# Kernel tuning notes

Hardware: AMD Instinct MI355X
Metric: run time of the kernel (lower is better)

Reference implementation:

```python
import jax, jax.numpy as jnp
import numpy as np

N_NODES = 100000
N_EDGES = 1600000
NFEAT, NHID, NCLASS = 64, 128, 32


def _glorot(key, shape):
    fan_in, fan_out = shape[0], shape[1]
    lim = np.sqrt(6.0 / (fan_in + fan_out))
    return jax.random.uniform(key, shape, jnp.float32, -lim, lim)


def setup_inputs() -> dict:
    key = jax.random.key(0)
    ks = jax.random.split(key, 12)
    x = jax.random.normal(ks[0], (N_NODES, NFEAT), jnp.float32)
    edge_idx = jax.random.randint(ks[1], (2, N_EDGES), 0, N_NODES, jnp.int64)
    edge_weight = jax.random.uniform(ks[2], (N_EDGES,), jnp.float32)
    return {
        "x": x,
        "edge_idx": edge_idx,
        "edge_weight": edge_weight,
        # SAGEConv 1: out = mean_agg(x) @ Wl1 + b1 + x @ Wr1
        "Wl1": _glorot(ks[3], (NFEAT, NHID)),
        "Wr1": _glorot(ks[4], (NFEAT, NHID)),
        "b1": jnp.zeros((NHID,), jnp.float32),
        # SAGEConv 2
        "Wl2": _glorot(ks[5], (NHID, NHID)),
        "Wr2": _glorot(ks[6], (NHID, NHID)),
        "b2": jnp.zeros((NHID,), jnp.float32),
        # fc head: Linear(nhid, nclass) -> Linear(nclass, 1)
        "Wfc1": _glorot(ks[7], (NHID, NCLASS)),
        "bfc1": jnp.zeros((NCLASS,), jnp.float32),
        "Wfc2": _glorot(ks[8], (NCLASS, 1)),
        "bfc2": jnp.zeros((1,), jnp.float32),
    }


def _sage_conv(x, src, dst, Wl, Wr, b, n_nodes):
    # mean aggregation of source features at destination nodes
    msg_sum = jax.ops.segment_sum(x[src], dst, num_segments=n_nodes)  # [N, d]
    deg = jax.ops.segment_sum(jnp.ones((src.shape[0], 1), x.dtype), dst,
                              num_segments=n_nodes)                    # [N, 1]
    mean = msg_sum / jnp.maximum(deg, 1.0)
    return mean @ Wl + b + x @ Wr


def reference(x, edge_idx, edge_weight, Wl1, Wr1, b1, Wl2, Wr2, b2,
              Wfc1, bfc1, Wfc2, bfc2):
    n_nodes = x.shape[0]
    src, dst = edge_idx[0], edge_idx[1]
    # dropout is identity in eval mode (training=False)
    h = _sage_conv(x, src, dst, Wl1, Wr1, b1, n_nodes)   # [N, nhid]
    h = _sage_conv(h, src, dst, Wl2, Wr2, b2, n_nodes)   # [N, nhid]
    h = h @ Wfc1 + bfc1                                   # [N, nclass]
    out = h @ Wfc2 + bfc2                                 # [N, 1]
    return out
```

## Files before the change

kernel.cpp:

```cpp
#include <hip/hip_runtime.h>

#define S_SHIFT 7
#define S_NODES 128
#define NBKT    784
#define CAP     2560
#define CHUNK   4096
#define NREP    4
#define TPB     256
#define TOTAL_BLOCKS 1024

__global__ __launch_bounds__(512) void prep_kernel(
    const float* __restrict__ Wl1, const float* __restrict__ Wr1, const float* __restrict__ b1,
    const float* __restrict__ Wl2, const float* __restrict__ Wr2, const float* __restrict__ b2,
    const float* __restrict__ Wfc1, const float* __restrict__ bfc1,
    const float* __restrict__ Wfc2, const float* __restrict__ bfc2,
    int* __restrict__ cursor, float* __restrict__ wv_g, float* __restrict__ c01)
{
    __shared__ float wv[192], uu[128], vl2[128], vr2[128], w2[32];
    int t = threadIdx.x;
    int l = t & 63;
    int w = t >> 6;
    for (int i = t; i < NBKT; i += 512) cursor[i] = 0;
    if (t < 32) w2[t] = Wfc2[t];
    __syncthreads();
    for (int j = 0; j < 16; ++j) {
        int i = w + 8 * j;
        float p = (l < 32) ? Wfc1[i * 32 + l] * w2[l] : 0.f;
        for (int m = 16; m; m >>= 1) p += __shfl_xor(p, m);
        if (l == 0) uu[i] = p;
    }
    __syncthreads();
    for (int j = 0; j < 16; ++j) {
        int i = w + 8 * j;
        float ua = uu[l], ub = uu[64 + l];
        float pa = Wl2[i * 128 + l] * ua + Wl2[i * 128 + 64 + l] * ub;
        float pb = Wr2[i * 128 + l] * ua + Wr2[i * 128 + 64 + l] * ub;
        for (int m = 32; m; m >>= 1) { pa += __shfl_xor(pa, m); pb += __shfl_xor(pb, m); }
        if (l == 0) { vl2[i] = pa; vr2[i] = pb; }
    }
    __syncthreads();
    for (int j = 0; j < 8; ++j) {
        int i = w + 8 * j;
        float l1a = Wl1[i * 128 + l], l1b = Wl1[i * 128 + 64 + l];
        float r1a = Wr1[i * 128 + l], r1b = Wr1[i * 128 + 64 + l];
        float La = vl2[l], Lb = vl2[64 + l], Ra = vr2[l], Rb = vr2[64 + l];
        float pc = l1a * La + l1b * Lb;
        float pb = l1a * Ra + l1b * Rb + r1a * La + r1b * Lb;
        float pa = r1a * Ra + r1b * Rb;
        for (int m = 32; m; m >>= 1) {
            pa += __shfl_xor(pa, m); pb += __shfl_xor(pb, m); pc += __shfl_xor(pc, m);
        }
        if (l == 0) { wv[i] = pa; wv[64 + i] = pb; wv[128 + i] = pc; }
    }
    if (w == 7) {
        float p0 = b1[l] * vr2[l] + b1[64 + l] * vr2[64 + l]
                 + b2[l] * uu[l] + b2[64 + l] * uu[64 + l];
        if (l < 32) p0 += bfc1[l] * w2[l];
        float p1 = b1[l] * vl2[l] + b1[64 + l] * vl2[64 + l];
        for (int m = 32; m; m >>= 1) { p0 += __shfl_xor(p0, m); p1 += __shfl_xor(p1, m); }
        if (l == 0) { c01[0] = p0 + bfc2[0]; c01[1] = p1; }
    }
    __syncthreads();
    for (int i = t; i < 192; i += 512) wv_g[i] = wv[i];
}

__global__ __launch_bounds__(TPB) void fused_kernel(
    const float* __restrict__ x,
    const int* __restrict__ src, const int* __restrict__ dst,
    int E, int N, int B, int nscat, int ndot,
    int* __restrict__ cursor, unsigned* __restrict__ bucket,
    const float* __restrict__ wv_g,
    float* __restrict__ ga, float2* __restrict__ gbc)
{
    __shared__ int hist[NBKT], lbase[NBKT], lcur[NBKT];
    int t = threadIdx.x;
    int l = t & 63;
    int w = t >> 6;
    int bid = blockIdx.x;

    if (bid < nscat) {
        int e0 = bid * CHUNK;
        int cnt = E - e0; if (cnt > CHUNK) cnt = CHUNK;
        for (int i = t; i < B; i += TPB) hist[i] = 0;
        __syncthreads();
        for (int i = t; i < cnt; i += TPB)
            atomicAdd(&hist[dst[e0 + i] >> S_SHIFT], 1);
        __syncthreads();
        for (int i = t; i < B; i += TPB) {
            lcur[i] = 0;
            if (hist[i] > 0) lbase[i] = atomicAdd(&cursor[i], hist[i]);
        }
        __syncthreads();
        for (int i = t; i < cnt; i += TPB) {
            int d = dst[e0 + i], s = src[e0 + i];
            int bb = d >> S_SHIFT;
            int off = atomicAdd(&lcur[bb], 1);
            bucket[(size_t)bb * CAP + (unsigned)(lbase[bb] + off)] =
                ((unsigned)s << S_SHIFT) | (unsigned)(d & (S_NODES - 1));
        }
    } else {
        int fp = l & 15, sub = l >> 4;
        float4 wa4 = ((const float4*)wv_g)[fp];
        float4 wb4 = ((const float4*)wv_g)[16 + fp];
        float4 wc4 = ((const float4*)wv_g)[32 + fp];
        const float4* x4 = (const float4*)x;
        int Q = (N + 3) >> 2;
        int wid = (bid - nscat) * (TPB / 64) + w;
        int stride = ndot * (TPB / 64);
        for (int qd = wid; qd < Q; qd += stride) {
            int node = qd * 4 + sub;
            float a = 0.f, b = 0.f, c = 0.f;
            if (node < N) {
                float4 v = x4[(size_t)node * 16 + fp];
                a = v.x * wa4.x + v.y * wa4.y + v.z * wa4.z + v.w * wa4.w;
                b = v.x * wb4.x + v.y * wb4.y + v.z * wb4.z + v.w * wb4.w;
                c = v.x * wc4.x + v.y * wc4.y + v.z * wc4.z + v.w * wc4.w;
            }
            for (int m = 8; m; m >>= 1) {
                a += __shfl_xor(a, m); b += __shfl_xor(b, m); c += __shfl_xor(c, m);
            }
            if (fp == 0 && node < N) { ga[node] = a; gbc[node] = make_float2(b, c); }
        }
    }
}

__global__ __launch_bounds__(TPB) void aggA_kernel(
    const unsigned* __restrict__ bucket, const int* __restrict__ cursor,
    const float2* __restrict__ gbc, const float* __restrict__ ga,
    const float* __restrict__ c01,
    float* __restrict__ q, float* __restrict__ t1, float* __restrict__ inv, int N)
{
    __shared__ float aB[NREP][S_NODES], aC[NREP][S_NODES];
    __shared__ int cnt[NREP][S_NODES];
    int t = threadIdx.x, b = blockIdx.x;
    int r = t >> 6;
    float* aBf = (float*)aB; float* aCf = (float*)aC; int* cnf = (int*)cnt;
    for (int i = t; i < NREP * S_NODES; i += TPB) { aBf[i] = 0.f; aCf[i] = 0.f; cnf[i] = 0; }
    __syncthreads();
    int n = cursor[b];
    const unsigned* bp = bucket + (size_t)b * CAP;
    int n4 = n & ~3;
    for (int i = 4 * t; i < n4; i += 4 * TPB) {
        uint4 e4 = *(const uint4*)(bp + i);
        float2 g0 = gbc[e4.x >> S_SHIFT];
        float2 g1 = gbc[e4.y >> S_SHIFT];
        float2 g2 = gbc[e4.z >> S_SHIFT];
        float2 g3 = gbc[e4.w >> S_SHIFT];
        int d0 = e4.x & (S_NODES - 1), d1 = e4.y & (S_NODES - 1);
        int d2 = e4.z & (S_NODES - 1), d3 = e4.w & (S_NODES - 1);
        atomicAdd(&aB[r][d0], g0.x); atomicAdd(&aC[r][d0], g0.y); atomicAdd(&cnt[r][d0], 1);
        atomicAdd(&aB[r][d1], g1.x); atomicAdd(&aC[r][d1], g1.y); atomicAdd(&cnt[r][d1], 1);
        atomicAdd(&aB[r][d2], g2.x); atomicAdd(&aC[r][d2], g2.y); atomicAdd(&cnt[r][d2], 1);
        atomicAdd(&aB[r][d3], g3.x); atomicAdd(&aC[r][d3], g3.y); atomicAdd(&cnt[r][d3], 1);
    }
    if (n4 + t < n) {
        unsigned uu = bp[n4 + t];
        float2 g = gbc[uu >> S_SHIFT];
        int dl = uu & (S_NODES - 1);
        atomicAdd(&aB[r][dl], g.x); atomicAdd(&aC[r][dl], g.y); atomicAdd(&cnt[r][dl], 1);
    }
    __syncthreads();
    if (t < S_NODES) {
        int node = (b << S_SHIFT) + t;
        if (node < N) {
            float sb = 0.f, sc = 0.f; int d = 0;
            #pragma unroll
            for (int k = 0; k < NREP; ++k) { sb += aB[k][t]; sc += aC[k][t]; d += cnt[k][t]; }
            float iv = 1.0f / ((d > 0) ? (float)d : 1.0f);
            inv[node] = iv;
            q[node]   = iv * sc;
            t1[node]  = ga[node] + iv * sb + c01[0] + (d > 0 ? c01[1] : 0.f);
        }
    }
}

__global__ __launch_bounds__(TPB) void aggB_kernel(
    const unsigned* __restrict__ bucket, const int* __restrict__ cursor,
    const float* __restrict__ q, const float* __restrict__ t1,
    const float* __restrict__ inv, float* __restrict__ out, int N)
{
    __shared__ float a2[NREP][S_NODES];
    int t = threadIdx.x, b = blockIdx.x;
    int r = t >> 6;
    float* a2f = (float*)a2;
    for (int i = t; i < NREP * S_NODES; i += TPB) a2f[i] = 0.f;
    __syncthreads();
    int n = cursor[b];
    const unsigned* bp = bucket + (size_t)b * CAP;
    int n4 = n & ~3;
    for (int i = 4 * t; i < n4; i += 4 * TPB) {
        uint4 e4 = *(const uint4*)(bp + i);
        float q0 = q[e4.x >> S_SHIFT], q1 = q[e4.y >> S_SHIFT];
        float q2 = q[e4.z >> S_SHIFT], q3 = q[e4.w >> S_SHIFT];
        atomicAdd(&a2[r][e4.x & (S_NODES - 1)], q0);
        atomicAdd(&a2[r][e4.y & (S_NODES - 1)], q1);
        atomicAdd(&a2[r][e4.z & (S_NODES - 1)], q2);
        atomicAdd(&a2[r][e4.w & (S_NODES - 1)], q3);
    }
    if (n4 + t < n) {
        unsigned uu = bp[n4 + t];
        atomicAdd(&a2[r][uu & (S_NODES - 1)], q[uu >> S_SHIFT]);
    }
    __syncthreads();
    if (t < S_NODES) {
        int node = (b << S_SHIFT) + t;
        if (node < N) {
            float s2 = 0.f;
            #pragma unroll
            for (int k = 0; k < NREP; ++k) s2 += a2[k][t];
            out[node] = t1[node] + inv[node] * s2;
        }
    }
}

extern "C" void kernel_launch(void* const* d_in, const int* in_sizes, int n_in,
                              void* d_out, int out_size, void* d_ws, size_t ws_size,
                              hipStream_t stream) {
    const float* x    = (const float*)d_in[0];
    const int*   eidx = (const int*)d_in[1];
    const float* Wl1  = (const float*)d_in[3];
    const float* Wr1  = (const float*)d_in[4];
    const float* b1   = (const float*)d_in[5];
    const float* Wl2  = (const float*)d_in[6];
    const float* Wr2  = (const float*)d_in[7];
    const float* b2   = (const float*)d_in[8];
    const float* Wfc1 = (const float*)d_in[9];
    const float* bfc1 = (const float*)d_in[10];
    const float* Wfc2 = (const float*)d_in[11];
    const float* bfc2 = (const float*)d_in[12];

    const int N = in_sizes[0] / 64;
    const int E = in_sizes[2];
    const int* src = eidx;
    const int* dst = eidx + E;
    const int B = (N + S_NODES - 1) >> S_SHIFT;
    const int nscat = (E + CHUNK - 1) / CHUNK;
    const int ndot = TOTAL_BLOCKS - nscat;

    char* ws = (char*)d_ws;
    int*      cursor = (int*)(ws);
    float*    wv_g   = (float*)(ws + 3136);
    float*    c01    = (float*)(ws + 3904);
    float*    ga     = (float*)(ws + 4096);
    float*    q      = (float*)(ws + 4096 + (size_t)N * 4);
    float*    t1     = (float*)(ws + 4096 + (size_t)N * 8);
    float*    inv    = (float*)(ws + 4096 + (size_t)N * 12);
    float2*   gbc    = (float2*)(ws + 4096 + (size_t)N * 16);
    unsigned* bucket = (unsigned*)(ws + 4096 + (size_t)N * 24);

    prep_kernel<<<1, 512, 0, stream>>>(Wl1, Wr1, b1, Wl2, Wr2, b2,
                                       Wfc1, bfc1, Wfc2, bfc2, cursor, wv_g, c01);

    fused_kernel<<<TOTAL_BLOCKS, TPB, 0, stream>>>(
        x, src, dst, E, N, B, nscat, ndot, cursor, bucket, wv_g, ga, gbc);

    aggA_kernel<<<B, TPB, 0, stream>>>(bucket, cursor, gbc, ga, c01, q, t1, inv, N);
    aggB_kernel<<<B, TPB, 0, stream>>>(bucket, cursor, q, t1, inv, (float*)d_out, N);
}
```

Before: 182.3 us.

## Fold weight-prep into fused kernel, memset cursors, prefetch bucket loads

Removes the single-block prep kernel. Every dot-product block now recomputes the collapsed weight vectors redundantly in shared memory, and the cursor reset becomes a memset. This cuts one serial launch and its tail latency, at the cost of repeated small matrix reductions per block. It also doubles the scatter chunk size, halving the number of scatter blocks, and adds one-ahead software prefetching of bucket entries in both aggregation kernels.

```diff
diff --git a/kernel.cpp b/kernel.cpp
--- a/kernel.cpp
+++ b/kernel.cpp
@@ -4,75 +4,25 @@
 #define S_NODES 128
 #define NBKT    784
 #define CAP     2560
-#define CHUNK   4096
+#define CHUNK   8192
 #define NREP    4
 #define TPB     256
 #define TOTAL_BLOCKS 1024
-
-__global__ __launch_bounds__(512) void prep_kernel(
-    const float* __restrict__ Wl1, const float* __restrict__ Wr1, const float* __restrict__ b1,
-    const float* __restrict__ Wl2, const float* __restrict__ Wr2, const float* __restrict__ b2,
-    const float* __restrict__ Wfc1, const float* __restrict__ bfc1,
-    const float* __restrict__ Wfc2, const float* __restrict__ bfc2,
-    int* __restrict__ cursor, float* __restrict__ wv_g, float* __restrict__ c01)
-{
-    __shared__ float wv[192], uu[128], vl2[128], vr2[128], w2[32];
-    int t = threadIdx.x;
-    int l = t & 63;
-    int w = t >> 6;
-    for (int i = t; i < NBKT; i += 512) cursor[i] = 0;
-    if (t < 32) w2[t] = Wfc2[t];
-    __syncthreads();
-    for (int j = 0; j < 16; ++j) {
-        int i = w + 8 * j;
-        float p = (l < 32) ? Wfc1[i * 32 + l] * w2[l] : 0.f;
-        for (int m = 16; m; m >>= 1) p += __shfl_xor(p, m);
-        if (l == 0) uu[i] = p;
-    }
-    __syncthreads();
-    for (int j = 0; j < 16; ++j) {
-        int i = w + 8 * j;
-        float ua = uu[l], ub = uu[64 + l];
-        float pa = Wl2[i * 128 + l] * ua + Wl2[i * 128 + 64 + l] * ub;
-        float pb = Wr2[i * 128 + l] * ua + Wr2[i * 128 + 64 + l] * ub;
-        for (int m = 32; m; m >>= 1) { pa += __shfl_xor(pa, m); pb += __shfl_xor(pb, m); }
-        if (l == 0) { vl2[i] = pa; vr2[i] = pb; }
-    }
-    __syncthreads();
-    for (int j = 0; j < 8; ++j) {
-        int i = w + 8 * j;
-        float l1a = Wl1[i * 128 + l], l1b = Wl1[i * 128 + 64 + l];
-        float r1a = Wr1[i * 128 + l], r1b = Wr1[i * 128 + 64 + l];
-        float La = vl2[l], Lb = vl2[64 + l], Ra = vr2[l], Rb = vr2[64 + l];
-        float pc = l1a * La + l1b * Lb;
-        float pb = l1a * Ra + l1b * Rb + r1a * La + r1b * Lb;
-        float pa = r1a * Ra + r1b * Rb;
-        for (int m = 32; m; m >>= 1) {
-            pa += __shfl_xor(pa, m); pb += __shfl_xor(pb, m); pc += __shfl_xor(pc, m);
-        }
-        if (l == 0) { wv[i] = pa; wv[64 + i] = pb; wv[128 + i] = pc; }
-    }
-    if (w == 7) {
-        float p0 = b1[l] * vr2[l] + b1[64 + l] * vr2[64 + l]
-                 + b2[l] * uu[l] + b2[64 + l] * uu[64 + l];
-        if (l < 32) p0 += bfc1[l] * w2[l];
-        float p1 = b1[l] * vl2[l] + b1[64 + l] * vl2[64 + l];
-        for (int m = 32; m; m >>= 1) { p0 += __shfl_xor(p0, m); p1 += __shfl_xor(p1, m); }
-        if (l == 0) { c01[0] = p0 + bfc2[0]; c01[1] = p1; }
-    }
-    __syncthreads();
-    for (int i = t; i < 192; i += 512) wv_g[i] = wv[i];
-}
 
 __global__ __launch_bounds__(TPB) void fused_kernel(
     const float* __restrict__ x,
     const int* __restrict__ src, const int* __restrict__ dst,
     int E, int N, int B, int nscat, int ndot,
     int* __restrict__ cursor, unsigned* __restrict__ bucket,
-    const float* __restrict__ wv_g,
-    float* __restrict__ ga, float2* __restrict__ gbc)
+    const float* __restrict__ Wl1, const float* __restrict__ Wr1, const float* __restrict__ b1,
+    const float* __restrict__ Wl2, const float* __restrict__ Wr2, const float* __restrict__ b2,
+    const float* __restrict__ Wfc1, const float* __restrict__ bfc1,
+    const float* __restrict__ Wfc2, const float* __restrict__ bfc2,
+    float* __restrict__ ga, float2* __restrict__ gbc, float* __restrict__ c01)
 {
     __shared__ int hist[NBKT], lbase[NBKT], lcur[NBKT];
+    __shared__ __align__(16) float wv[192];
+    __shared__ float uu[128], vl2[128], vr2[128], w2[32];
     int t = threadIdx.x;
     int l = t & 63;
     int w = t >> 6;
@@ -99,10 +49,51 @@
                 ((unsigned)s << S_SHIFT) | (unsigned)(d & (S_NODES - 1));
         }
     } else {
+        if (t < 32) w2[t] = Wfc2[t];
+        __syncthreads();
+        for (int j = 0; j < 32; ++j) {
+            int i = w + 4 * j;
+            float p = (l < 32) ? Wfc1[i * 32 + l] * w2[l] : 0.f;
+            for (int m = 16; m; m >>= 1) p += __shfl_xor(p, m);
+            if (l == 0) uu[i] = p;
+        }
+        __syncthreads();
+        for (int j = 0; j < 32; ++j) {
+            int i = w + 4 * j;
+            float ua = uu[l], ub = uu[64 + l];
+            float pa = Wl2[i * 128 + l] * ua + Wl2[i * 128 + 64 + l] * ub;
+            float pb = Wr2[i * 128 + l] * ua + Wr2[i * 128 + 64 + l] * ub;
+            for (int m = 32; m; m >>= 1) { pa += __shfl_xor(pa, m); pb += __shfl_xor(pb, m); }
+            if (l == 0) { vl2[i] = pa; vr2[i] = pb; }
+        }
+        __syncthreads();
+        for (int j = 0; j < 16; ++j) {
+            int i = w + 4 * j;
+            float l1a = Wl1[i * 128 + l], l1b = Wl1[i * 128 + 64 + l];
+            float r1a = Wr1[i * 128 + l], r1b = Wr1[i * 128 + 64 + l];
+            float La = vl2[l], Lb = vl2[64 + l], Ra = vr2[l], Rb = vr2[64 + l];
+            float pc = l1a * La + l1b * Lb;
+            float pb = l1a * Ra + l1b * Rb + r1a * La + r1b * Lb;
+            float pa = r1a * Ra + r1b * Rb;
+            for (int m = 32; m; m >>= 1) {
+                pa += __shfl_xor(pa, m); pb += __shfl_xor(pb, m); pc += __shfl_xor(pc, m);
+            }
+            if (l == 0) { wv[i] = pa; wv[64 + i] = pb; wv[128 + i] = pc; }
+        }
+        if (bid == nscat && w == 3) {
+            float p0 = b1[l] * vr2[l] + b1[64 + l] * vr2[64 + l]
+                     + b2[l] * uu[l] + b2[64 + l] * uu[64 + l];
+            if (l < 32) p0 += bfc1[l] * w2[l];
+            float p1 = b1[l] * vl2[l] + b1[64 + l] * vl2[64 + l];
+            for (int m = 32; m; m >>= 1) { p0 += __shfl_xor(p0, m); p1 += __shfl_xor(p1, m); }
+            if (l == 0) { c01[0] = p0 + bfc2[0]; c01[1] = p1; }
+        }
+        __syncthreads();
+
         int fp = l & 15, sub = l >> 4;
-        float4 wa4 = ((const float4*)wv_g)[fp];
-        float4 wb4 = ((const float4*)wv_g)[16 + fp];
-        float4 wc4 = ((const float4*)wv_g)[32 + fp];
+        float4 wa4 = ((const float4*)wv)[fp];
+        float4 wb4 = ((const float4*)wv)[16 + fp];
+        float4 wc4 = ((const float4*)wv)[32 + fp];
         const float4* x4 = (const float4*)x;
         int Q = (N + 3) >> 2;
         int wid = (bid - nscat) * (TPB / 64) + w;
@@ -140,18 +131,26 @@
     int n = cursor[b];
     const unsigned* bp = bucket + (size_t)b * CAP;
     int n4 = n & ~3;
-    for (int i = 4 * t; i < n4; i += 4 * TPB) {
-        uint4 e4 = *(const uint4*)(bp + i);
-        float2 g0 = gbc[e4.x >> S_SHIFT];
-        float2 g1 = gbc[e4.y >> S_SHIFT];
-        float2 g2 = gbc[e4.z >> S_SHIFT];
-        float2 g3 = gbc[e4.w >> S_SHIFT];
-        int d0 = e4.x & (S_NODES - 1), d1 = e4.y & (S_NODES - 1);
-        int d2 = e4.z & (S_NODES - 1), d3 = e4.w & (S_NODES - 1);
+    int i = 4 * t;
+    bool have = i < n4;
+    uint4 cur = make_uint4(0, 0, 0, 0);
+    if (have) cur = *(const uint4*)(bp + i);
+    while (have) {
+        int in2 = i + 4 * TPB;
+        bool hn = in2 < n4;
+        uint4 nxt = cur;
+        if (hn) nxt = *(const uint4*)(bp + in2);
+        float2 g0 = gbc[cur.x >> S_SHIFT];
+        float2 g1 = gbc[cur.y >> S_SHIFT];
+        float2 g2 = gbc[cur.z >> S_SHIFT];
+        float2 g3 = gbc[cur.w >> S_SHIFT];
+        int d0 = cur.x & (S_NODES - 1), d1 = cur.y & (S_NODES - 1);
+        int d2 = cur.z & (S_NODES - 1), d3 = cur.w & (S_NODES - 1);
         atomicAdd(&aB[r][d0], g0.x); atomicAdd(&aC[r][d0], g0.y); atomicAdd(&cnt[r][d0], 1);
         atomicAdd(&aB[r][d1], g1.x); atomicAdd(&aC[r][d1], g1.y); atomicAdd(&cnt[r][d1], 1);
         atomicAdd(&aB[r][d2], g2.x); atomicAdd(&aC[r][d2], g2.y); atomicAdd(&cnt[r][d2], 1);
         atomicAdd(&aB[r][d3], g3.x); atomicAdd(&aC[r][d3], g3.y); atomicAdd(&cnt[r][d3], 1);
+        cur = nxt; i = in2; have = hn;
     }
     if (n4 + t < n) {
         unsigned uu = bp[n4 + t];
@@ -188,14 +187,22 @@
     int n = cursor[b];
     const unsigned* bp = bucket + (size_t)b * CAP;
     int n4 = n & ~3;
-    for (int i = 4 * t; i < n4; i += 4 * TPB) {
-        uint4 e4 = *(const uint4*)(bp + i);
-        float q0 = q[e4.x >> S_SHIFT], q1 = q[e4.y >> S_SHIFT];
-        float q2 = q[e4.z >> S_SHIFT], q3 = q[e4.w >> S_SHIFT];
-        atomicAdd(&a2[r][e4.x & (S_NODES - 1)], q0);
-        atomicAdd(&a2[r][e4.y & (S_NODES - 1)], q1);
-        atomicAdd(&a2[r][e4.z & (S_NODES - 1)], q2);
-        atomicAdd(&a2[r][e4.w & (S_NODES - 1)], q3);
+    int i = 4 * t;
+    bool have = i < n4;
+    uint4 cur = make_uint4(0, 0, 0, 0);
+    if (have) cur = *(const uint4*)(bp + i);
+    while (have) {
+        int in2 = i + 4 * TPB;
+        bool hn = in2 < n4;
+        uint4 nxt = cur;
+        if (hn) nxt = *(const uint4*)(bp + in2);
+        float q0 = q[cur.x >> S_SHIFT], q1 = q[cur.y >> S_SHIFT];
+        float q2 = q[cur.z >> S_SHIFT], q3 = q[cur.w >> S_SHIFT];
+        atomicAdd(&a2[r][cur.x & (S_NODES - 1)], q0);
+        atomicAdd(&a2[r][cur.y & (S_NODES - 1)], q1);
+        atomicAdd(&a2[r][cur.z & (S_NODES - 1)], q2);
+        atomicAdd(&a2[r][cur.w & (S_NODES - 1)], q3);
+        cur = nxt; i = in2; have = hn;
     }
     if (n4 + t < n) {
         unsigned uu = bp[n4 + t];
@@ -239,8 +246,7 @@
 
     char* ws = (char*)d_ws;
     int*      cursor = (int*)(ws);
-    float*    wv_g   = (float*)(ws + 3136);
-    float*    c01    = (float*)(ws + 3904);
+    float*    c01    = (float*)(ws + 3200);
     float*    ga     = (float*)(ws + 4096);
     float*    q      = (float*)(ws + 4096 + (size_t)N * 4);
     float*    t1     = (float*)(ws + 4096 + (size_t)N * 8);
@@ -248,11 +254,12 @@
     float2*   gbc    = (float2*)(ws + 4096 + (size_t)N * 16);
     unsigned* bucket = (unsigned*)(ws + 4096 + (size_t)N * 24);
 
-    prep_kernel<<<1, 512, 0, stream>>>(Wl1, Wr1, b1, Wl2, Wr2, b2,
-                                       Wfc1, bfc1, Wfc2, bfc2, cursor, wv_g, c01);
+    hipMemsetAsync(cursor, 0, 3136, stream);
 
     fused_kernel<<<TOTAL_BLOCKS, TPB, 0, stream>>>(
-        x, src, dst, E, N, B, nscat, ndot, cursor, bucket, wv_g, ga, gbc);
+        x, src, dst, E, N, B, nscat, ndot, cursor, bucket,
+        Wl1, Wr1, b1, Wl2, Wr2, b2, Wfc1, bfc1, Wfc2, bfc2,
+        ga, gbc, c01);
 
     aggA_kernel<<<B, TPB, 0, stream>>>(bucket, cursor, gbc, ga, c01, q, t1, inv, N);
     aggB_kernel<<<B, TPB, 0, stream>>>(bucket, cursor, q, t1, inv, (float*)d_out, N);
```

New measurement: 196.4 us. 1.08x slower.
